# Optimization experiments

Hardware: AMD Instinct MI355X
Metric: run time of the kernel (lower is better)

## Reference

```python
import jax, jax.numpy as jnp
import numpy as np

N = 4194304

def _unit_hemisphere(key, n):
    v = jax.random.normal(key, (n, 3), dtype=jnp.float32)
    v = v / jnp.linalg.norm(v, axis=-1, keepdims=True)
    # keep directions in the upper hemisphere (normal = +z) as in BRDF fitting data
    return v.at[:, 2].set(jnp.abs(v[:, 2]) + 1e-3)

def setup_inputs() -> dict:
    key = jax.random.key(0)
    k1, k2 = jax.random.split(key)
    light = _unit_hemisphere(k1, N)
    view = _unit_hemisphere(k2, N)
    inputs = jnp.stack([light, view], axis=1)  # [N, 2, 3]
    return {
        "inputs": inputs,
        "base_color": jnp.array([0.8, 0.8, 0.8], dtype=jnp.float32),
        "alpha": jnp.array([0.25], dtype=jnp.float32),
        "eta": jnp.array([1.45], dtype=jnp.float32),
    }

def _forward(inputs, base_color, alpha, eta):
    light = inputs[:, 0, :]  # [N,3]
    view = inputs[:, 1, :]   # [N,3]
    h = light + view
    h = h / jnp.linalg.norm(h, axis=-1, keepdims=True)

    cos_nh = h[:, 2]                      # normal = (0,0,1)
    cos_hv = jnp.sum(h * view, axis=-1)
    cos_nl = light[:, 2]
    cos_nv = view[:, 2]

    # D: GGX/Trowbridge-Reitz NDF (base class returns 0; standard subclass NDF used)
    a2 = alpha[0] * alpha[0]
    dd = cos_nh * cos_nh * (a2 - 1.0) + 1.0
    D = a2 / (jnp.pi * dd * dd)

    # F: exact Cook-Torrance Fresnel with data-dependent branch as where
    c = cos_hv
    g2 = eta[0] * eta[0] + c * c - 1.0
    g = jnp.sqrt(jnp.maximum(g2, 1e-12))
    a = (g - c) / (g + c)
    b = (c * (g + c) - 1.0) / (c * (g - c) + 1.0)
    F = jnp.where(g2 > 0.0, 0.5 * a * a * (1.0 + b * b), 1.0)

    # G: as in module's g(): dot(n,l) * dot(n,v)
    G = cos_nl * cos_nv

    lin = jnp.power(base_color, 2.2)  # mon2lin: sRGB-ish gamma to linear
    scale = D * G * F / (4.0 * cos_nl * cos_nv)
    return lin[None, :] * scale[:, None]  # [N,3]

def reference(inputs, base_color, alpha, eta):
    return _forward(inputs, base_color, alpha, eta)
```

## Files before the change

kernel.cpp:

```cpp
#include <hip/hip_runtime.h>
#include <math.h>


__device__ __forceinline__ float brdf_scale(
    float lx, float ly, float lz,
    float vx, float vy, float vz,
    float a2, float eta2)
{
    float hx = lx + vx, hy = ly + vy, hz = lz + vz;
    float rn = __builtin_amdgcn_rsqf(hx * hx + hy * hy + hz * hz);
    hx *= rn; hy *= rn; hz *= rn;

    float cos_nh = hz;
    float c = hx * vx + hy * vy + hz * vz;

    float dd = cos_nh * cos_nh * (a2 - 1.0f) + 1.0f;
    float D = a2 * __builtin_amdgcn_rcpf(3.14159274f * dd * dd);

    float g2 = eta2 + c * c - 1.0f;
    float g = sqrtf(fmaxf(g2, 1e-12f));
    float a = (g - c) * __builtin_amdgcn_rcpf(g + c);
    float b = (c * (g + c) - 1.0f) * __builtin_amdgcn_rcpf(c * (g - c) + 1.0f);
    float F = (g2 > 0.0f) ? (0.5f * a * a * (1.0f + b * b)) : 1.0f;

    return D * F * 0.25f;
}

__global__ __launch_bounds__(256) void microfacet_kernel(
    const float* __restrict__ in,
    const float* __restrict__ base_color,
    const float* __restrict__ alpha,
    const float* __restrict__ eta,
    float* __restrict__ out,
    int nquads)
{
    const float al = alpha[0];
    const float a2 = al * al;
    const float et = eta[0];
    const float eta2 = et * et;
    const float lin0 = powf(base_color[0], 2.2f);
    const float lin1 = powf(base_color[1], 2.2f);
    const float lin2 = powf(base_color[2], 2.2f);

    const float4* __restrict__ in4 = (const float4*)in;
    float4* __restrict__ out4 = (float4*)out;

    const int j = blockIdx.x * blockDim.x + threadIdx.x;
    if (j >= nquads) return;
    const int i6 = 6 * j;

    float4 q0 = in4[i6 + 0];
    float4 q1 = in4[i6 + 1];
    float4 q2 = in4[i6 + 2];
    float4 q3 = in4[i6 + 3];
    float4 q4 = in4[i6 + 4];
    float4 q5 = in4[i6 + 5];

    float s0 = brdf_scale(q0.x, q0.y, q0.z, q0.w, q1.x, q1.y, a2, eta2);
    float s1 = brdf_scale(q1.z, q1.w, q2.x, q2.y, q2.z, q2.w, a2, eta2);
    float s2 = brdf_scale(q3.x, q3.y, q3.z, q3.w, q4.x, q4.y, a2, eta2);
    float s3 = brdf_scale(q4.z, q4.w, q5.x, q5.y, q5.z, q5.w, a2, eta2);

    const int o3 = 3 * j;
    out4[o3 + 0] = make_float4(lin0 * s0, lin1 * s0, lin2 * s0, lin0 * s1);
    out4[o3 + 1] = make_float4(lin1 * s1, lin2 * s1, lin0 * s2, lin1 * s2);
    out4[o3 + 2] = make_float4(lin2 * s2, lin0 * s3, lin1 * s3, lin2 * s3);
}

extern "C" void kernel_launch(void* const* d_in, const int* in_sizes, int n_in,
                              void* d_out, int out_size, void* d_ws, size_t ws_size,
                              hipStream_t stream) {
    const float* in = (const float*)d_in[0];
    const float* base_color = (const float*)d_in[1];
    const float* alpha = (const float*)d_in[2];
    const float* eta = (const float*)d_in[3];
    float* out = (float*)d_out;

    const int n = in_sizes[0] / 6;
    const int nquads = n / 4;

    const int block = 256;
    const int grid = (nquads + block - 1) / block;
    microfacet_kernel<<<grid, block, 0, stream>>>(in, base_color, alpha, eta,
                                                  out, nquads);
}
```

Before: 165.6 us.

## Stage input and output through LDS for fully coalesced float4 accesses

New measurement: 164.9 us. About the same (-0.4%).

```diff
diff --git a/kernel.cpp b/kernel.cpp
--- a/kernel.cpp
+++ b/kernel.cpp
@@ -27,13 +27,19 @@
 }
 
 __global__ __launch_bounds__(256) void microfacet_kernel(
-    const float* __restrict__ in,
+    const float4* __restrict__ in4,
     const float* __restrict__ base_color,
     const float* __restrict__ alpha,
     const float* __restrict__ eta,
-    float* __restrict__ out,
-    int nquads)
+    float4* __restrict__ out4,
+    int n_in4, int n_out4)
 {
+    __shared__ float4 lds[768];
+
+    const int tid = threadIdx.x;
+    const int in_base  = blockIdx.x * 768;
+    const int out_base = blockIdx.x * 384;
+
     const float al = alpha[0];
     const float a2 = al * al;
     const float et = eta[0];
@@ -42,45 +48,56 @@
     const float lin1 = powf(base_color[1], 2.2f);
     const float lin2 = powf(base_color[2], 2.2f);
 
-    const float4* __restrict__ in4 = (const float4*)in;
-    float4* __restrict__ out4 = (float4*)out;
+#pragma unroll
+    for (int k = 0; k < 3; ++k) {
+        const int g = in_base + k * 256 + tid;
+        lds[k * 256 + tid] = (g < n_in4) ? in4[g] : make_float4(0.f, 0.f, 0.f, 1.f);
+    }
+    __syncthreads();
 
-    const int j = blockIdx.x * blockDim.x + threadIdx.x;
-    if (j >= nquads) return;
-    const int i6 = 6 * j;
+    const float4 q0 = lds[3 * tid + 0];
+    const float4 q1 = lds[3 * tid + 1];
+    const float4 q2 = lds[3 * tid + 2];
 
-    float4 q0 = in4[i6 + 0];
-    float4 q1 = in4[i6 + 1];
-    float4 q2 = in4[i6 + 2];
-    float4 q3 = in4[i6 + 3];
-    float4 q4 = in4[i6 + 4];
-    float4 q5 = in4[i6 + 5];
+    const float sA = brdf_scale(q0.x, q0.y, q0.z, q0.w, q1.x, q1.y, a2, eta2);
+    const float sB = brdf_scale(q1.z, q1.w, q2.x, q2.y, q2.z, q2.w, a2, eta2);
 
-    float s0 = brdf_scale(q0.x, q0.y, q0.z, q0.w, q1.x, q1.y, a2, eta2);
-    float s1 = brdf_scale(q1.z, q1.w, q2.x, q2.y, q2.z, q2.w, a2, eta2);
-    float s2 = brdf_scale(q3.x, q3.y, q3.z, q3.w, q4.x, q4.y, a2, eta2);
-    float s3 = brdf_scale(q4.z, q4.w, q5.x, q5.y, q5.z, q5.w, a2, eta2);
+    __syncthreads();
 
-    const int o3 = 3 * j;
-    out4[o3 + 0] = make_float4(lin0 * s0, lin1 * s0, lin2 * s0, lin0 * s1);
-    out4[o3 + 1] = make_float4(lin1 * s1, lin2 * s1, lin0 * s2, lin1 * s2);
-    out4[o3 + 2] = make_float4(lin2 * s2, lin0 * s3, lin1 * s3, lin2 * s3);
+    float* lf = (float*)lds;
+    lf[6 * tid + 0] = lin0 * sA;
+    lf[6 * tid + 1] = lin1 * sA;
+    lf[6 * tid + 2] = lin2 * sA;
+    lf[6 * tid + 3] = lin0 * sB;
+    lf[6 * tid + 4] = lin1 * sB;
+    lf[6 * tid + 5] = lin2 * sB;
+    __syncthreads();
+
+    {
+        const int g = out_base + tid;
+        if (g < n_out4) out4[g] = lds[tid];
+        if (tid < 128) {
+            const int g2 = out_base + 256 + tid;
+            if (g2 < n_out4) out4[g2] = lds[256 + tid];
+        }
+    }
 }
 
 extern "C" void kernel_launch(void* const* d_in, const int* in_sizes, int n_in,
                               void* d_out, int out_size, void* d_ws, size_t ws_size,
                               hipStream_t stream) {
-    const float* in = (const float*)d_in[0];
+    const float4* in4 = (const float4*)d_in[0];
     const float* base_color = (const float*)d_in[1];
     const float* alpha = (const float*)d_in[2];
     const float* eta = (const float*)d_in[3];
-    float* out = (float*)d_out;
+    float4* out4 = (float4*)d_out;
 
     const int n = in_sizes[0] / 6;
-    const int nquads = n / 4;
+    const int n_in4 = in_sizes[0] / 4;
+    const int n_out4 = out_size / 4;
 
     const int block = 256;
-    const int grid = (nquads + block - 1) / block;
-    microfacet_kernel<<<grid, block, 0, stream>>>(in, base_color, alpha, eta,
-                                                  out, nquads);
+    const int grid = (n + 511) / 512;
+    microfacet_kernel<<<grid, block, 0, stream>>>(in4, base_color, alpha, eta,
+                                                  out4, n_in4, n_out4);
 }
```
